# Kernel optimization log

Hardware: AMD Instinct MI355X
Metric: run time of the kernel (lower is better)

The kernel has to match this reference:

```python
import jax, jax.numpy as jnp
import numpy as np

N = 50000
E = 800000
IN_CH, CDK, EDGE_DIM = 40, 200, 10
HID, HEADS = 64, 4
NEG_SLOPE = 0.2
SM_EPS = 1e-16
BN_EPS = 1e-5


def _glorot(key, shape):
    fan = shape[0] + shape[-1]
    return jax.random.normal(key, shape, jnp.float32) * jnp.sqrt(2.0 / fan)


def setup_inputs() -> dict:
    key = jax.random.key(0)
    ks = iter(jax.random.split(key, 40))
    inp = {
        'x': jax.random.normal(next(ks), (N, IN_CH), jnp.float32),
        'cdk_desc': jax.random.normal(next(ks), (N, CDK), jnp.float32),
        'edge_src': jax.random.randint(next(ks), (E,), 0, N, jnp.int32),
        'edge_dst': jax.random.randint(next(ks), (E,), 0, N, jnp.int32),
        'edge_attr': jax.random.normal(next(ks), (E, EDGE_DIM), jnp.float32),
    }
    dims = [(IN_CH + CDK, HEADS, HID), (HID * HEADS, HEADS, HID), (HID * HEADS, 1, HID)]
    for i, (din, h, c) in enumerate(dims):
        inp[f'W{i}'] = _glorot(next(ks), (din, h * c))
        inp[f'as{i}'] = _glorot(next(ks), (h, c))
        inp[f'ad{i}'] = _glorot(next(ks), (h, c))
        inp[f'We{i}'] = _glorot(next(ks), (EDGE_DIM, h * c))
        inp[f'ae{i}'] = _glorot(next(ks), (h, c))
        inp[f'b{i}'] = jnp.zeros((h * c,), jnp.float32)
        inp[f'g{i}'] = jnp.ones((h * c,), jnp.float32)
        inp[f'be{i}'] = jnp.zeros((h * c,), jnp.float32)
    inp['linW'] = _glorot(next(ks), (HID, 1))
    inp['linB'] = jnp.zeros((1,), jnp.float32)
    return inp


def gat_conv(x, src, dst, ea, W, a_s, a_d, We, a_e, b, heads, c):
    # PyG GATConv: shared linear for src/dst, edge features, segment softmax.
    xp = (x @ W).reshape(N, heads, c)                 # [N,H,C]
    ep = (ea @ We).reshape(-1, heads, c)              # [Etot,H,C]
    al_s = (xp * a_s).sum(-1)                         # [N,H]
    al_d = (xp * a_d).sum(-1)                         # [N,H]
    al_e = (ep * a_e).sum(-1)                         # [Etot,H]
    alpha = jax.nn.leaky_relu(al_s[src] + al_d[dst] + al_e, NEG_SLOPE)
    m = jax.ops.segment_max(alpha, dst, num_segments=N)
    ex = jnp.exp(alpha - m[dst])
    den = jax.ops.segment_sum(ex, dst, num_segments=N)
    att = ex / (den[dst] + SM_EPS)                    # [Etot,H]
    out = jax.ops.segment_sum(xp[src] * att[:, :, None], dst, num_segments=N)
    return out.reshape(N, heads * c) + b


def batch_norm(x, g, be):
    mu = x.mean(0)
    var = x.var(0)
    return g * (x - mu) * jax.lax.rsqrt(var + BN_EPS) + be


def reference(x, cdk_desc, edge_src, edge_dst, edge_attr,
              W0, as0, ad0, We0, ae0, b0, g0, be0,
              W1, as1, ad1, We1, ae1, b1, g1, be1,
              W2, as2, ad2, We2, ae2, b2, g2, be2,
              linW, linB):
    # add self-loops once (PyG default add_self_loops=True, fill_value='mean')
    loop = jnp.arange(N, dtype=edge_src.dtype)
    src = jnp.concatenate([edge_src, loop])
    dst = jnp.concatenate([edge_dst, loop])
    ea_mean = edge_attr.mean(0)
    ea = jnp.concatenate([edge_attr, jnp.broadcast_to(ea_mean, (N, EDGE_DIM))], 0)

    h = jnp.concatenate([x, cdk_desc], axis=-1)
    layers = [
        (W0, as0, ad0, We0, ae0, b0, g0, be0, HEADS),
        (W1, as1, ad1, We1, ae1, b1, g1, be1, HEADS),
        (W2, as2, ad2, We2, ae2, b2, g2, be2, 1),
    ]
    for (W, a_s, a_d, We, a_e, b, g, be, heads) in layers:
        h = gat_conv(h, src, dst, ea, W, a_s, a_d, We, a_e, b, heads, HID)
        h = batch_norm(h, g, be)
        h = jax.nn.elu(h)
        # dropout is identity in eval mode
    out = h @ linW + linB
    return jax.nn.sigmoid(out).squeeze(-1)
```

## Files before the change

kernel.cpp:

```cpp
#include <hip/hip_runtime.h>
#include <math.h>

#define NNODES 50000
#define NEDGES 800000
#define ETOT   (NNODES + NEDGES)
#define EDIM   10
#define SMEPS  1e-16f
#define BNEPS  1e-5f
#define NSLOPE 0.2f

#define SCANB  ((NNODES + 255) / 256)
#define EASUMB 256
#define BNB    256

typedef _Float16 f16;
typedef f16 f16x8 __attribute__((ext_vector_type(8)));
typedef f16 f16x4 __attribute__((ext_vector_type(4)));
typedef float f32x4 __attribute__((ext_vector_type(4)));


__global__ void k_deg(const int* __restrict__ edst, int* __restrict__ deg) {
    int e = blockIdx.x * blockDim.x + threadIdx.x;
    if (e >= ETOT) return;
    int d = (e < NEDGES) ? edst[e] : (e - NEDGES);
    atomicAdd(&deg[d], 1);
}

__global__ void k_easum(const float* __restrict__ ea, float* __restrict__ part) {
    float acc[EDIM];
#pragma unroll
    for (int d = 0; d < EDIM; ++d) acc[d] = 0.f;
    int tid = blockIdx.x * blockDim.x + threadIdx.x;
    const int np = NEDGES / 2;
    for (int p = tid; p < np; p += gridDim.x * blockDim.x) {
        const float4* q = (const float4*)&ea[(long)p * 20];
        float4 v0 = q[0], v1 = q[1], v2 = q[2], v3 = q[3], v4 = q[4];
        acc[0] += v0.x + v2.z;
        acc[1] += v0.y + v2.w;
        acc[2] += v0.z + v3.x;
        acc[3] += v0.w + v3.y;
        acc[4] += v1.x + v3.z;
        acc[5] += v1.y + v3.w;
        acc[6] += v1.z + v4.x;
        acc[7] += v1.w + v4.y;
        acc[8] += v2.x + v4.z;
        acc[9] += v2.y + v4.w;
    }
    __shared__ float sm[256];
    for (int d = 0; d < EDIM; ++d) {
        sm[threadIdx.x] = acc[d];
        __syncthreads();
        for (int s = 128; s > 0; s >>= 1) {
            if (threadIdx.x < s) sm[threadIdx.x] += sm[threadIdx.x + s];
            __syncthreads();
        }
        if (threadIdx.x == 0) part[blockIdx.x * EDIM + d] = sm[0];
        __syncthreads();
    }
}

__global__ void k_scan1(const int* __restrict__ deg, int* __restrict__ off,
                        int* __restrict__ partials) {
    __shared__ int sm[256];
    int t = threadIdx.x;
    int i = blockIdx.x * 256 + t;
    int v = (i < NNODES) ? deg[i] : 0;
    sm[t] = v;
    __syncthreads();
    int val = v;
    for (int d = 1; d < 256; d <<= 1) {
        int tv = (t >= d) ? sm[t - d] : 0;
        __syncthreads();
        val += tv;
        sm[t] = val;
        __syncthreads();
    }
    if (i < NNODES) off[i] = val - v;
    if (t == 255) partials[blockIdx.x] = val;
}

__global__ void k_scan2(int* __restrict__ partials, int* __restrict__ off) {
    __shared__ int sm[256];
    int t = threadIdx.x;
    int v = (t < SCANB) ? partials[t] : 0;
    sm[t] = v;
    __syncthreads();
    int val = v;
    for (int d = 1; d < 256; d <<= 1) {
        int tv = (t >= d) ? sm[t - d] : 0;
        __syncthreads();
        val += tv;
        sm[t] = val;
        __syncthreads();
    }
    if (t < SCANB) partials[t] = val - v;
    if (t == 255) off[NNODES] = ETOT;
}

__global__ void k_scan3(int* __restrict__ off, const int* __restrict__ partials) {
    int i = blockIdx.x * 256 + threadIdx.x;
    if (i < NNODES) off[i] += partials[blockIdx.x];
}

__global__ void k_scatter(const int* __restrict__ esrc, const int* __restrict__ edst,
                          const int* __restrict__ off, int* __restrict__ cursor,
                          int* __restrict__ csr_src, int* __restrict__ perm) {
    int e = blockIdx.x * blockDim.x + threadIdx.x;
    if (e >= ETOT) return;
    int s, d;
    if (e < NEDGES) { s = esrc[e]; d = edst[e]; }
    else            { s = d = e - NEDGES; }
    int pos  = atomicAdd(&cursor[d], 1);
    int slot = off[d] + pos;
    csr_src[slot] = s;
    perm[e] = slot;
}

__global__ void k_concat_h(const float* __restrict__ x, const float* __restrict__ cdk,
                           f16* __restrict__ out) {
    int i = blockIdx.x * blockDim.x + threadIdx.x;
    if (i >= NNODES * 256) return;
    int n = i >> 8, j = i & 255;
    float v = (j < 40) ? x[n * 40 + j] : (j < 240) ? cdk[n * 200 + (j - 40)] : 0.f;
    out[i] = (f16)v;
}

__global__ void k_wcvt_all(const float* __restrict__ W0, const float* __restrict__ W1,
                           const float* __restrict__ W2, f16* __restrict__ Wt0,
                           f16* __restrict__ Wt1, f16* __restrict__ Wt2) {
    int i = blockIdx.x * blockDim.x + threadIdx.x;
    const float* W; f16* Wt; int K, NC, j;
    if (i < 65536)       { W = W0; Wt = Wt0; K = 240; NC = 256; j = i; }
    else if (i < 131072) { W = W1; Wt = Wt1; K = 256; NC = 256; j = i - 65536; }
    else if (i < 147456) { W = W2; Wt = Wt2; K = 256; NC = 64;  j = i - 131072; }
    else return;
    int n = j >> 8, k = j & 255;
    Wt[j] = (k < K) ? (f16)W[k * NC + n] : (f16)0.f;
}

#define GM_LDS 40
__global__ __launch_bounds__(256) void k_gemm_h(const f16* __restrict__ A,
                                                const f16* __restrict__ Bt,
                                                f16* __restrict__ C,
                                                const float* __restrict__ a_s,
                                                const float* __restrict__ a_d,
                                                float* __restrict__ als,
                                                float* __restrict__ ald,
                                                int M, int NC, int H) {
    __shared__ f16 As[128 * GM_LDS];
    __shared__ f16 Bs[64 * GM_LDS];
    const int t    = threadIdx.x;
    const int w    = t >> 6;
    const int lane = t & 63;
    const int row0 = blockIdx.x * 128;
    const int col0 = blockIdx.y * 64;

    const int ar = t >> 1;
    const int ak = (t & 1) * 16;
    const int bn = t >> 2;
    const int bk = (t & 3) * 8;

    const int l16 = lane & 15;
    const int kg  = lane >> 4;

    f32x4 acc[2][4];
#pragma unroll
    for (int i = 0; i < 2; ++i)
#pragma unroll
        for (int j = 0; j < 4; ++j) acc[i][j] = {0.f, 0.f, 0.f, 0.f};

    for (int k0 = 0; k0 < 256; k0 += 32) {
        f16x8 av0, av1;
#pragma unroll
        for (int i = 0; i < 8; ++i) { av0[i] = (f16)0.f; av1[i] = (f16)0.f; }
        if (row0 + ar < M) {
            const f16* ap = &A[(long)(row0 + ar) * 256 + k0 + ak];
            av0 = *(const f16x8*)ap;
            av1 = *(const f16x8*)(ap + 8);
        }
        *(f16x8*)&As[ar * GM_LDS + ak]     = av0;
        *(f16x8*)&As[ar * GM_LDS + ak + 8] = av1;
        f16x8 bv = *(const f16x8*)&Bt[(long)(col0 + bn) * 256 + k0 + bk];
        *(f16x8*)&Bs[bn * GM_LDS + bk] = bv;
        __syncthreads();

        f16x8 afr[2], bfr[4];
#pragma unroll
        for (int mi = 0; mi < 2; ++mi)
            afr[mi] = *(const f16x8*)&As[(w * 32 + mi * 16 + l16) * GM_LDS + kg * 8];
#pragma unroll
        for (int ni = 0; ni < 4; ++ni)
            bfr[ni] = *(const f16x8*)&Bs[(ni * 16 + l16) * GM_LDS + kg * 8];
#pragma unroll
        for (int mi = 0; mi < 2; ++mi)
#pragma unroll
            for (int ni = 0; ni < 4; ++ni)
                acc[mi][ni] = __builtin_amdgcn_mfma_f32_16x16x32_f16(
                    afr[mi], bfr[ni], acc[mi][ni], 0, 0, 0);
        __syncthreads();
    }

#pragma unroll
    for (int mi = 0; mi < 2; ++mi)
#pragma unroll
        for (int ni = 0; ni < 4; ++ni)
#pragma unroll
            for (int j = 0; j < 4; ++j) {
                int r = row0 + w * 32 + mi * 16 + kg * 4 + j;
                if (r < M) C[(long)r * NC + col0 + ni * 16 + l16] = (f16)acc[mi][ni][j];
            }

    const int hidx = blockIdx.y;
    float asv[4], adv[4];
#pragma unroll
    for (int ni = 0; ni < 4; ++ni) {
        asv[ni] = a_s[hidx * 64 + ni * 16 + l16];
        adv[ni] = a_d[hidx * 64 + ni * 16 + l16];
    }
#pragma unroll
    for (int mi = 0; mi < 2; ++mi)
#pragma unroll
        for (int j = 0; j < 4; ++j) {
            float ps = acc[mi][0][j] * asv[0] + acc[mi][1][j] * asv[1]
                     + acc[mi][2][j] * asv[2] + acc[mi][3][j] * asv[3];
            float pd = acc[mi][0][j] * adv[0] + acc[mi][1][j] * adv[1]
                     + acc[mi][2][j] * adv[2] + acc[mi][3][j] * adv[3];
#pragma unroll
            for (int o = 1; o < 16; o <<= 1) {
                ps += __shfl_xor(ps, o);
                pd += __shfl_xor(pd, o);
            }
            int r = row0 + w * 32 + mi * 16 + kg * 4 + j;
            if (l16 == 0 && r < M) {
                als[(long)r * H + hidx] = ps;
                ald[(long)r * H + hidx] = pd;
            }
        }
}

__global__ void k_ve_all(const float* __restrict__ We0, const float* __restrict__ ae0,
                         const float* __restrict__ We1, const float* __restrict__ ae1,
                         const float* __restrict__ We2, const float* __restrict__ ae2,
                         const float* __restrict__ eapart,
                         float* __restrict__ VeAll, float* __restrict__ laAll) {
    int l = blockIdx.x;
    const float* We = (l == 0) ? We0 : (l == 1) ? We1 : We2;
    const float* ae = (l == 0) ? ae0 : (l == 1) ? ae1 : ae2;
    int H = (l == 2) ? 1 : 4;
    float* Ve = VeAll + l * 48;
    float* la = laAll + l * 4;
    int t = threadIdx.x;

    float ac[EDIM];
#pragma unroll
    for (int d = 0; d < EDIM; ++d) ac[d] = 0.f;
    for (int r = t; r < EASUMB; r += 64) {
#pragma unroll
        for (int d = 0; d < EDIM; ++d) ac[d] += eapart[r * EDIM + d];
    }
#pragma unroll
    for (int o = 1; o < 64; o <<= 1) {
#pragma unroll
        for (int d = 0; d < EDIM; ++d) ac[d] += __shfl_xor(ac[d], o);
    }

    if (t < EDIM * H) {
        int d = t / H, h = t % H;
        float s = 0.f;
        for (int c = 0; c < 64; ++c) s += We[d * (H * 64) + h * 64 + c] * ae[h * 64 + c];
        Ve[d * H + h] = s;
    }
    __syncthreads();
    if (t < H) {
        float s = 0.f;
        for (int d = 0; d < EDIM; ++d) s += (ac[d] * (1.0f / NEDGES)) * Ve[d * H + t];
        la[t] = s;
    }
}

template <int H>
__global__ void k_edge(const float* __restrict__ ea, const int* __restrict__ esrc,
                       const int* __restrict__ edst, const float* __restrict__ als,
                       const float* __restrict__ ald, const float* __restrict__ Ve,
                       const float* __restrict__ loop_al, const int* __restrict__ perm,
                       f16* __restrict__ alpha) {
    int e = blockIdx.x * blockDim.x + threadIdx.x;
    if (e >= ETOT) return;
    int s, d;
    float ale[H];
    if (e < NEDGES) {
        s = esrc[e]; d = edst[e];
#pragma unroll
        for (int h = 0; h < H; ++h) ale[h] = 0.f;
#pragma unroll
        for (int dd = 0; dd < EDIM; ++dd) {
            float v = ea[(long)e * EDIM + dd];
#pragma unroll
            for (int h = 0; h < H; ++h) ale[h] = fmaf(v, Ve[dd * H + h], ale[h]);
        }
    } else {
        s = d = e - NEDGES;
#pragma unroll
        for (int h = 0; h < H; ++h) ale[h] = loop_al[h];
    }
    int slot = perm[e];
#pragma unroll
    for (int h = 0; h < H; ++h) {
        float a = als[s * H + h] + ald[d * H + h] + ale[h];
        a = (a > 0.f) ? a : NSLOPE * a;
        alpha[(long)slot * H + h] = (f16)a;
    }
}

template <int H>
__global__ __launch_bounds__(256) void k_agg(const f16* __restrict__ xp,
                                             const f16* __restrict__ alpha,
                                             const int* __restrict__ off,
                                             const int* __restrict__ csr_src,
                                             f16* __restrict__ out) {
    int gw   = (blockIdx.x * blockDim.x + threadIdx.x) >> 6;
    int lane = threadIdx.x & 63;
    if (gw >= NNODES) return;
    int o0 = off[gw], o1 = off[gw + 1];

    if constexpr (H == 4) {
        constexpr int T = 4;
        int h  = lane >> 4;
        int il = lane & 15;
        int glane = lane & 48;

        float av[T];
        int   idx[T];
        float mx = -INFINITY;
#pragma unroll
        for (int t = 0; t < T; ++t) {
            int s = o0 + t * 16 + il;
            bool ok = (s < o1);
            float a = ok ? (float)alpha[(long)s * 4 + h] : -INFINITY;
            idx[t] = ok ? csr_src[s] : 0;
            av[t] = a;
            mx = fmaxf(mx, a);
        }
        for (int s = o0 + T * 16 + il; s < o1; s += 16)
            mx = fmaxf(mx, (float)alpha[(long)s * 4 + h]);
#pragma unroll
        for (int o = 1; o < 16; o <<= 1) mx = fmaxf(mx, __shfl_xor(mx, o));

        float den = 0.f;
#pragma unroll
        for (int t = 0; t < T; ++t) {
            float e = expf(av[t] - mx);
            av[t] = e;
            den += e;
        }
        for (int s = o0 + T * 16 + il; s < o1; s += 16)
            den += expf((float)alpha[(long)s * 4 + h] - mx);
#pragma unroll
        for (int o = 1; o < 16; o <<= 1) den += __shfl_xor(den, o);
        float di = 1.0f / (den + SMEPS);

        float4 acc0 = make_float4(0.f, 0.f, 0.f, 0.f);
        float4 acc1 = make_float4(0.f, 0.f, 0.f, 0.f);
#pragma unroll
        for (int t = 0; t < T; ++t) {
            int base = o0 + t * 16;
            if (base >= o1) break;
            int cnt = min(16, o1 - base);
            int j = 0;
            for (; j + 4 <= cnt; j += 4) {
                float w0 = __shfl(av[t],  glane + j,     64);
                int  sn0 = __shfl(idx[t], glane + j,     64);
                float w1 = __shfl(av[t],  glane + j + 1, 64);
                int  sn1 = __shfl(idx[t], glane + j + 1, 64);
                float w2 = __shfl(av[t],  glane + j + 2, 64);
                int  sn2 = __shfl(idx[t], glane + j + 2, 64);
                float w3 = __shfl(av[t],  glane + j + 3, 64);
                int  sn3 = __shfl(idx[t], glane + j + 3, 64);
                f16x4 x0 = *(const f16x4*)&xp[(long)sn0 * 256 + lane * 4];
                f16x4 x1 = *(const f16x4*)&xp[(long)sn1 * 256 + lane * 4];
                f16x4 x2 = *(const f16x4*)&xp[(long)sn2 * 256 + lane * 4];
                f16x4 x3 = *(const f16x4*)&xp[(long)sn3 * 256 + lane * 4];
                acc0.x = fmaf(w0, (float)x0[0], acc0.x);
                acc0.y = fmaf(w0, (float)x0[1], acc0.y);
                acc0.z = fmaf(w0, (float)x0[2], acc0.z);
                acc0.w = fmaf(w0, (float)x0[3], acc0.w);
                acc1.x = fmaf(w1, (float)x1[0], acc1.x);
                acc1.y = fmaf(w1, (float)x1[1], acc1.y);
                acc1.z = fmaf(w1, (float)x1[2], acc1.z);
                acc1.w = fmaf(w1, (float)x1[3], acc1.w);
                acc0.x = fmaf(w2, (float)x2[0], acc0.x);
                acc0.y = fmaf(w2, (float)x2[1], acc0.y);
                acc0.z = fmaf(w2, (float)x2[2], acc0.z);
                acc0.w = fmaf(w2, (float)x2[3], acc0.w);
                acc1.x = fmaf(w3, (float)x3[0], acc1.x);
                acc1.y = fmaf(w3, (float)x3[1], acc1.y);
                acc1.z = fmaf(w3, (float)x3[2], acc1.z);
                acc1.w = fmaf(w3, (float)x3[3], acc1.w);
            }
            for (; j < cnt; ++j) {
                float w  = __shfl(av[t],  glane + j, 64);
                int   sn = __shfl(idx[t], glane + j, 64);
                f16x4 xh = *(const f16x4*)&xp[(long)sn * 256 + lane * 4];
                acc0.x = fmaf(w, (float)xh[0], acc0.x);
                acc0.y = fmaf(w, (float)xh[1], acc0.y);
                acc0.z = fmaf(w, (float)xh[2], acc0.z);
                acc0.w = fmaf(w, (float)xh[3], acc0.w);
            }
        }
        for (int s = o0 + T * 16; s < o1; ++s) {
            float w  = expf((float)alpha[(long)s * 4 + h] - mx);
            int   sn = csr_src[s];
            f16x4 xh = *(const f16x4*)&xp[(long)sn * 256 + lane * 4];
            acc0.x = fmaf(w, (float)xh[0], acc0.x);
            acc0.y = fmaf(w, (float)xh[1], acc0.y);
            acc0.z = fmaf(w, (float)xh[2], acc0.z);
            acc0.w = fmaf(w, (float)xh[3], acc0.w);
        }
        f16x4 o4 = {(f16)((acc0.x + acc1.x) * di), (f16)((acc0.y + acc1.y) * di),
                    (f16)((acc0.z + acc1.z) * di), (f16)((acc0.w + acc1.w) * di)};
        *(f16x4*)&out[(long)gw * 256 + lane * 4] = o4;
    } else {
        constexpr int T = 2;
        float av[T];
        int   idx[T];
        float mx = -INFINITY;
#pragma unroll
        for (int t = 0; t < T; ++t) {
            int s = o0 + t * 64 + lane;
            bool ok = (s < o1);
            float a = ok ? (float)alpha[s] : -INFINITY;
            idx[t] = ok ? csr_src[s] : 0;
            av[t] = a;
            mx = fmaxf(mx, a);
        }
        for (int s = o0 + T * 64 + lane; s < o1; s += 64)
            mx = fmaxf(mx, (float)alpha[s]);
#pragma unroll
        for (int o = 1; o < 64; o <<= 1) mx = fmaxf(mx, __shfl_xor(mx, o));

        float den = 0.f;
#pragma unroll
        for (int t = 0; t < T; ++t) {
            float e = expf(av[t] - mx);
            av[t] = e;
            den += e;
        }
        for (int s = o0 + T * 64 + lane; s < o1; s += 64)
            den += expf((float)alpha[s] - mx);
#pragma unroll
        for (int o = 1; o < 64; o <<= 1) den += __shfl_xor(den, o);
        float di = 1.0f / (den + SMEPS);

        float acc0 = 0.f, acc1 = 0.f;
#pragma unroll
        for (int t = 0; t < T; ++t) {
            int base = o0 + t * 64;
            if (base >= o1) break;
            int c2 = min(64, o1 - base);
            int j = 0;
            for (; j + 4 <= c2; j += 4) {
                float w0 = __shfl(av[t],  j,     64);
                int  sn0 = __shfl(idx[t], j,     64);
                float w1 = __shfl(av[t],  j + 1, 64);
                int  sn1 = __shfl(idx[t], j + 1, 64);
                float w2 = __shfl(av[t],  j + 2, 64);
                int  sn2 = __shfl(idx[t], j + 2, 64);
                float w3 = __shfl(av[t],  j + 3, 64);
                int  sn3 = __shfl(idx[t], j + 3, 64);
                float x0 = (float)xp[(long)sn0 * 64 + lane];
                float x1 = (float)xp[(long)sn1 * 64 + lane];
                float x2 = (float)xp[(long)sn2 * 64 + lane];
                float x3 = (float)xp[(long)sn3 * 64 + lane];
                acc0 = fmaf(w0, x0, acc0);
                acc1 = fmaf(w1, x1, acc1);
                acc0 = fmaf(w2, x2, acc0);
                acc1 = fmaf(w3, x3, acc1);
            }
            for (; j < c2; ++j) {
                float w  = __shfl(av[t],  j, 64);
                int   sn = __shfl(idx[t], j, 64);
                acc0 = fmaf(w, (float)xp[(long)sn * 64 + lane], acc0);
            }
        }
        for (int s = o0 + T * 64; s < o1; ++s) {
            float w  = expf((float)alpha[s] - mx);
            int   sn = csr_src[s];
            acc0 = fmaf(w, (float)xp[(long)sn * 64 + lane], acc0);
        }
        out[(long)gw * 64 + lane] = (f16)((acc0 + acc1) * di);
    }
}

__global__ void k_bnstats(const f16* __restrict__ x, int width,
                          float* __restrict__ s1p, float* __restrict__ s2p) {
    __shared__ float sa[256], sb[256];
    int col  = threadIdx.x % width;
    int rsub = threadIdx.x / width;
    int rpb  = 256 / width;
    float a = 0.f, b = 0.f;
    for (int r = blockIdx.x * rpb + rsub; r < NNODES; r += gridDim.x * rpb) {
        float v = (float)x[(long)r * width + col];
        a += v; b += v * v;
    }
    if (rpb == 1) {
        s1p[blockIdx.x * width + col] = a;
        s2p[blockIdx.x * width + col] = b;
    } else {
        sa[threadIdx.x] = a;
        sb[threadIdx.x] = b;
        __syncthreads();
        if (rsub == 0) {
            for (int k = 1; k < rpb; ++k) {
                a += sa[col + k * width];
                b += sb[col + k * width];
            }
            s1p[blockIdx.x * width + col] = a;
            s2p[blockIdx.x * width + col] = b;
        }
    }
}

__global__ void k_bnfin(const float* __restrict__ s1p, const float* __restrict__ s2p,
                        const float* __restrict__ g, const float* __restrict__ be,
                        int width, float* __restrict__ scale, float* __restrict__ shift) {
    int c = threadIdx.x;
    if (c >= width) return;
    float s1 = 0.f, s2 = 0.f;
    for (int k = 0; k < BNB; ++k) {
        s1 += s1p[k * width + c];
        s2 += s2p[k * width + c];
    }
    float mu  = s1 * (1.0f / NNODES);
    float var = s2 * (1.0f / NNODES) - mu * mu;
    float sc  = g[c] * rsqrtf(var + BNEPS);
    scale[c] = sc;
    shift[c] = be[c] - mu * sc;
}

__global__ void k_bnelu_h(const f16* __restrict__ xin, f16* __restrict__ xout,
                          const float* __restrict__ scale, const float* __restrict__ shift,
                          int width) {
    long i = (long)(blockIdx.x * blockDim.x + threadIdx.x);
    long total = (long)NNODES * width;
    if (i * 4 >= total) return;
    f16x4 v4 = *(const f16x4*)&xin[i * 4];
    int c = (int)((i * 4) % width);
    float4 sc = *(const float4*)&scale[c];
    float4 sh = *(const float4*)&shift[c];
    float y0 = (float)v4[0] * sc.x + sh.x;
    float y1 = (float)v4[1] * sc.y + sh.y;
    float y2 = (float)v4[2] * sc.z + sh.z;
    float y3 = (float)v4[3] * sc.w + sh.w;
    y0 = (y0 > 0.f) ? y0 : expm1f(y0);
    y1 = (y1 > 0.f) ? y1 : expm1f(y1);
    y2 = (y2 > 0.f) ? y2 : expm1f(y2);
    y3 = (y3 > 0.f) ? y3 : expm1f(y3);
    f16x4 o = {(f16)y0, (f16)y1, (f16)y2, (f16)y3};
    *(f16x4*)&xout[i * 4] = o;
}

__global__ __launch_bounds__(256) void k_final(const f16* __restrict__ h,
                                               const float* __restrict__ linW,
                                               const float* __restrict__ linB,
                                               float* __restrict__ out) {
    int gw   = (blockIdx.x * blockDim.x + threadIdx.x) >> 6;
    int lane = threadIdx.x & 63;
    if (gw >= NNODES) return;
    float v = (float)h[(long)gw * 64 + lane] * linW[lane];
    for (int o = 32; o > 0; o >>= 1) v += __shfl_xor(v, o);
    if (lane == 0) out[gw] = 1.0f / (1.0f + expf(-(v + linB[0])));
}

extern "C" void kernel_launch(void* const* d_in, const int* in_sizes, int n_in,
                              void* d_out, int out_size, void* d_ws, size_t ws_size,
                              hipStream_t stream) {
    (void)in_sizes; (void)n_in; (void)out_size; (void)ws_size;
    const float* x    = (const float*)d_in[0];
    const float* cdk  = (const float*)d_in[1];
    const int*   esrc = (const int*)d_in[2];
    const int*   edst = (const int*)d_in[3];
    const float* ea   = (const float*)d_in[4];
    const float* W[3]   = {(const float*)d_in[5],  (const float*)d_in[13], (const float*)d_in[21]};
    const float* as_[3] = {(const float*)d_in[6],  (const float*)d_in[14], (const float*)d_in[22]};
    const float* ad_[3] = {(const float*)d_in[7],  (const float*)d_in[15], (const float*)d_in[23]};
    const float* We_[3] = {(const float*)d_in[8],  (const float*)d_in[16], (const float*)d_in[24]};
    const float* ae_[3] = {(const float*)d_in[9],  (const float*)d_in[17], (const float*)d_in[25]};
    const float* g_[3]  = {(const float*)d_in[11], (const float*)d_in[19], (const float*)d_in[27]};
    const float* be_[3] = {(const float*)d_in[12], (const float*)d_in[20], (const float*)d_in[28]};
    const float* linW = (const float*)d_in[29];
    const float* linB = (const float*)d_in[30];
    float* out = (float*)d_out;

    char* base = (char*)d_ws;
    size_t p = 0;
    auto alloc = [&](size_t bytes) -> void* {
        void* r = base + p;
        p = (p + bytes + 255) & ~(size_t)255;
        return r;
    };
    int*   deg     = (int*)alloc((size_t)NNODES * 4);
    int*   cursor  = (int*)alloc((size_t)NNODES * 4);
    size_t zero_bytes = p;
    int*   off     = (int*)alloc((size_t)(NNODES + 1) * 4);
    int*   partials= (int*)alloc((size_t)SCANB * 4);
    float* eapart  = (float*)alloc((size_t)EASUMB * EDIM * 4);
    float* s1p     = (float*)alloc((size_t)BNB * 256 * 4);
    float* s2p     = (float*)alloc((size_t)BNB * 256 * 4);
    int*   csr_src = (int*)alloc((size_t)ETOT * 4);
    int*   perm    = (int*)alloc((size_t)ETOT * 4);
    f16*   alpha   = (f16*)alloc((size_t)ETOT * 4 * 2);
    float* als     = (float*)alloc((size_t)NNODES * 4 * 4);
    float* ald     = (float*)alloc((size_t)NNODES * 4 * 4);
    float* VeAll   = (float*)alloc((size_t)3 * 48 * 4);
    float* laAll   = (float*)alloc((size_t)3 * 4 * 4);
    float* scale   = (float*)alloc(256 * 4);
    float* shift   = (float*)alloc(256 * 4);
    f16*   Wt[3];
    Wt[0]          = (f16*)alloc((size_t)256 * 256 * 2);
    Wt[1]          = (f16*)alloc((size_t)256 * 256 * 2);
    Wt[2]          = (f16*)alloc((size_t)64 * 256 * 2);
    f16*   bufA_h  = (f16*)alloc((size_t)NNODES * 256 * 2);
    f16*   bufXp_h = (f16*)alloc((size_t)NNODES * 256 * 2);
    f16*   bufC_h  = (f16*)alloc((size_t)NNODES * 256 * 2);

    hipMemsetAsync(base, 0, zero_bytes, stream);

    int eb = (ETOT + 255) / 256;
    k_deg<<<eb, 256, 0, stream>>>(edst, deg);
    k_easum<<<EASUMB, 256, 0, stream>>>(ea, eapart);
    k_scan1<<<SCANB, 256, 0, stream>>>(deg, off, partials);
    k_scan2<<<1, 256, 0, stream>>>(partials, off);
    k_scan3<<<SCANB, 256, 0, stream>>>(off, partials);
    k_scatter<<<eb, 256, 0, stream>>>(esrc, edst, off, cursor, csr_src, perm);
    k_concat_h<<<(NNODES * 256 + 255) / 256, 256, 0, stream>>>(x, cdk, bufA_h);
    k_wcvt_all<<<576, 256, 0, stream>>>(W[0], W[1], W[2], Wt[0], Wt[1], Wt[2]);
    k_ve_all<<<3, 64, 0, stream>>>(We_[0], ae_[0], We_[1], ae_[1], We_[2], ae_[2],
                                   eapart, VeAll, laAll);

    const int nodeblocks = (NNODES * 64) / 256;
    const int mblocks = (NNODES + 127) / 128;

    for (int l = 0; l < 3; ++l) {
        const int H  = (l == 2) ? 1 : 4;
        const int NC = H * 64;
        const float* Ve  = VeAll + l * 48;
        const float* la  = laAll + l * 4;
        dim3 gg(mblocks, NC / 64);
        k_gemm_h<<<gg, 256, 0, stream>>>(bufA_h, Wt[l], bufXp_h,
                                         as_[l], ad_[l], als, ald, NNODES, NC, H);
        if (H == 4) {
            k_edge<4><<<eb, 256, 0, stream>>>(ea, esrc, edst, als, ald, Ve, la, perm, alpha);
            k_agg<4><<<nodeblocks, 256, 0, stream>>>(bufXp_h, alpha, off, csr_src, bufC_h);
        } else {
            k_edge<1><<<eb, 256, 0, stream>>>(ea, esrc, edst, als, ald, Ve, la, perm, alpha);
            k_agg<1><<<nodeblocks, 256, 0, stream>>>(bufXp_h, alpha, off, csr_src, bufC_h);
        }
        k_bnstats<<<BNB, 256, 0, stream>>>(bufC_h, NC, s1p, s2p);
        k_bnfin<<<1, 256, 0, stream>>>(s1p, s2p, g_[l], be_[l], NC, scale, shift);
        k_bnelu_h<<<(NNODES * NC / 4 + 255) / 256, 256, 0, stream>>>(bufC_h, bufA_h, scale, shift, NC);
    }
    k_final<<<nodeblocks, 256, 0, stream>>>(bufA_h, linW, linB, out);
}
```

Baseline: 631.8 us.

## Replace CSR build with fixed-capacity per-node edge slots plus overflow list

```diff
diff --git a/kernel.cpp b/kernel.cpp
--- a/kernel.cpp
+++ b/kernel.cpp
@@ -9,21 +9,35 @@
 #define BNEPS  1e-5f
 #define NSLOPE 0.2f
 
-#define SCANB  ((NNODES + 255) / 256)
 #define EASUMB 256
 #define BNB    256
+#define CAP    64
 
 typedef _Float16 f16;
 typedef f16 f16x8 __attribute__((ext_vector_type(8)));
 typedef f16 f16x4 __attribute__((ext_vector_type(4)));
 typedef float f32x4 __attribute__((ext_vector_type(4)));
 
-
-__global__ void k_deg(const int* __restrict__ edst, int* __restrict__ deg) {
+__global__ void k_place(const int* __restrict__ esrc, const int* __restrict__ edst,
+                        int* __restrict__ deg, int* __restrict__ csr_src,
+                        int* __restrict__ perm, int* __restrict__ ovf_cnt,
+                        int* __restrict__ ovf_src, int* __restrict__ ovf_dst) {
     int e = blockIdx.x * blockDim.x + threadIdx.x;
     if (e >= ETOT) return;
-    int d = (e < NEDGES) ? edst[e] : (e - NEDGES);
-    atomicAdd(&deg[d], 1);
+    int s, d;
+    if (e < NEDGES) { s = esrc[e]; d = edst[e]; }
+    else            { s = d = e - NEDGES; }
+    int pos = atomicAdd(&deg[d], 1);
+    if (pos < CAP) {
+        int slot = d * CAP + pos;
+        csr_src[slot] = s;
+        perm[e] = slot;
+    } else {
+        int k = atomicAdd(ovf_cnt, 1);
+        ovf_src[k] = s;
+        ovf_dst[k] = d;
+        perm[e] = -1 - k;
+    }
 }
 
 __global__ void k_easum(const float* __restrict__ ea, float* __restrict__ part) {
@@ -59,63 +73,6 @@
     }
 }
 
-__global__ void k_scan1(const int* __restrict__ deg, int* __restrict__ off,
-                        int* __restrict__ partials) {
-    __shared__ int sm[256];
-    int t = threadIdx.x;
-    int i = blockIdx.x * 256 + t;
-    int v = (i < NNODES) ? deg[i] : 0;
-    sm[t] = v;
-    __syncthreads();
-    int val = v;
-    for (int d = 1; d < 256; d <<= 1) {
-        int tv = (t >= d) ? sm[t - d] : 0;
-        __syncthreads();
-        val += tv;
-        sm[t] = val;
-        __syncthreads();
-    }
-    if (i < NNODES) off[i] = val - v;
-    if (t == 255) partials[blockIdx.x] = val;
-}
-
-__global__ void k_scan2(int* __restrict__ partials, int* __restrict__ off) {
-    __shared__ int sm[256];
-    int t = threadIdx.x;
-    int v = (t < SCANB) ? partials[t] : 0;
-    sm[t] = v;
-    __syncthreads();
-    int val = v;
-    for (int d = 1; d < 256; d <<= 1) {
-        int tv = (t >= d) ? sm[t - d] : 0;
-        __syncthreads();
-        val += tv;
-        sm[t] = val;
-        __syncthreads();
-    }
-    if (t < SCANB) partials[t] = val - v;
-    if (t == 255) off[NNODES] = ETOT;
-}
-
-__global__ void k_scan3(int* __restrict__ off, const int* __restrict__ partials) {
-    int i = blockIdx.x * 256 + threadIdx.x;
-    if (i < NNODES) off[i] += partials[blockIdx.x];
-}
-
-__global__ void k_scatter(const int* __restrict__ esrc, const int* __restrict__ edst,
-                          const int* __restrict__ off, int* __restrict__ cursor,
-                          int* __restrict__ csr_src, int* __restrict__ perm) {
-    int e = blockIdx.x * blockDim.x + threadIdx.x;
-    if (e >= ETOT) return;
-    int s, d;
-    if (e < NEDGES) { s = esrc[e]; d = edst[e]; }
-    else            { s = d = e - NEDGES; }
-    int pos  = atomicAdd(&cursor[d], 1);
-    int slot = off[d] + pos;
-    csr_src[slot] = s;
-    perm[e] = slot;
-}
-
 __global__ void k_concat_h(const float* __restrict__ x, const float* __restrict__ cdk,
                            f16* __restrict__ out) {
     int i = blockIdx.x * blockDim.x + threadIdx.x;
@@ -283,7 +240,7 @@
                        const int* __restrict__ edst, const float* __restrict__ als,
                        const float* __restrict__ ald, const float* __restrict__ Ve,
                        const float* __restrict__ loop_al, const int* __restrict__ perm,
-                       f16* __restrict__ alpha) {
+                       f16* __restrict__ alpha, f16* __restrict__ alpha_ovf) {
     int e = blockIdx.x * blockDim.x + threadIdx.x;
     if (e >= ETOT) return;
     int s, d;
@@ -304,24 +261,34 @@
         for (int h = 0; h < H; ++h) ale[h] = loop_al[h];
     }
     int slot = perm[e];
+    f16* dst = (slot >= 0) ? &alpha[(long)slot * H]
+                           : &alpha_ovf[(long)(-1 - slot) * H];
 #pragma unroll
     for (int h = 0; h < H; ++h) {
         float a = als[s * H + h] + ald[d * H + h] + ale[h];
         a = (a > 0.f) ? a : NSLOPE * a;
-        alpha[(long)slot * H + h] = (f16)a;
+        dst[h] = (f16)a;
     }
 }
 
 template <int H>
 __global__ __launch_bounds__(256) void k_agg(const f16* __restrict__ xp,
                                              const f16* __restrict__ alpha,
-                                             const int* __restrict__ off,
+                                             const int* __restrict__ deg,
                                              const int* __restrict__ csr_src,
+                                             const int* __restrict__ ovf_cnt,
+                                             const int* __restrict__ ovf_src,
+                                             const int* __restrict__ ovf_dst,
+                                             const f16* __restrict__ alpha_ovf,
                                              f16* __restrict__ out) {
     int gw   = (blockIdx.x * blockDim.x + threadIdx.x) >> 6;
     int lane = threadIdx.x & 63;
     if (gw >= NNODES) return;
-    int o0 = off[gw], o1 = off[gw + 1];
+    int dcount = deg[gw];
+    int cnt = min(dcount, CAP);
+    int o0 = gw * CAP;
+    int o1 = o0 + cnt;
+    bool ovf = (dcount > CAP);
 
     if constexpr (H == 4) {
         constexpr int T = 4;
@@ -341,10 +308,14 @@
             av[t] = a;
             mx = fmaxf(mx, a);
         }
-        for (int s = o0 + T * 16 + il; s < o1; s += 16)
-            mx = fmaxf(mx, (float)alpha[(long)s * 4 + h]);
 #pragma unroll
         for (int o = 1; o < 16; o <<= 1) mx = fmaxf(mx, __shfl_xor(mx, o));
+        if (ovf) {
+            int nov = *ovf_cnt;
+            for (int k = 0; k < nov; ++k)
+                if (ovf_dst[k] == gw)
+                    mx = fmaxf(mx, (float)alpha_ovf[(long)k * 4 + h]);
+        }
 
         float den = 0.f;
 #pragma unroll
@@ -353,21 +324,25 @@
             av[t] = e;
             den += e;
         }
-        for (int s = o0 + T * 16 + il; s < o1; s += 16)
-            den += expf((float)alpha[(long)s * 4 + h] - mx);
 #pragma unroll
         for (int o = 1; o < 16; o <<= 1) den += __shfl_xor(den, o);
+        if (ovf) {
+            int nov = *ovf_cnt;
+            for (int k = 0; k < nov; ++k)
+                if (ovf_dst[k] == gw)
+                    den += expf((float)alpha_ovf[(long)k * 4 + h] - mx);
+        }
         float di = 1.0f / (den + SMEPS);
 
         float4 acc0 = make_float4(0.f, 0.f, 0.f, 0.f);
         float4 acc1 = make_float4(0.f, 0.f, 0.f, 0.f);
 #pragma unroll
         for (int t = 0; t < T; ++t) {
-            int base = o0 + t * 16;
-            if (base >= o1) break;
-            int cnt = min(16, o1 - base);
+            int base = t * 16;
+            if (base >= cnt) break;
+            int c2 = min(16, cnt - base);
             int j = 0;
-            for (; j + 4 <= cnt; j += 4) {
+            for (; j + 4 <= c2; j += 4) {
                 float w0 = __shfl(av[t],  glane + j,     64);
                 int  sn0 = __shfl(idx[t], glane + j,     64);
                 float w1 = __shfl(av[t],  glane + j + 1, 64);
@@ -397,7 +372,7 @@
                 acc1.z = fmaf(w3, (float)x3[2], acc1.z);
                 acc1.w = fmaf(w3, (float)x3[3], acc1.w);
             }
-            for (; j < cnt; ++j) {
+            for (; j < c2; ++j) {
                 float w  = __shfl(av[t],  glane + j, 64);
                 int   sn = __shfl(idx[t], glane + j, 64);
                 f16x4 xh = *(const f16x4*)&xp[(long)sn * 256 + lane * 4];
@@ -407,85 +382,83 @@
                 acc0.w = fmaf(w, (float)xh[3], acc0.w);
             }
         }
-        for (int s = o0 + T * 16; s < o1; ++s) {
-            float w  = expf((float)alpha[(long)s * 4 + h] - mx);
-            int   sn = csr_src[s];
-            f16x4 xh = *(const f16x4*)&xp[(long)sn * 256 + lane * 4];
-            acc0.x = fmaf(w, (float)xh[0], acc0.x);
-            acc0.y = fmaf(w, (float)xh[1], acc0.y);
-            acc0.z = fmaf(w, (float)xh[2], acc0.z);
-            acc0.w = fmaf(w, (float)xh[3], acc0.w);
+        if (ovf) {
+            int nov = *ovf_cnt;
+            for (int k = 0; k < nov; ++k) {
+                if (ovf_dst[k] == gw) {
+                    float w  = expf((float)alpha_ovf[(long)k * 4 + h] - mx);
+                    int   sn = ovf_src[k];
+                    f16x4 xh = *(const f16x4*)&xp[(long)sn * 256 + lane * 4];
+                    acc0.x = fmaf(w, (float)xh[0], acc0.x);
+                    acc0.y = fmaf(w, (float)xh[1], acc0.y);
+                    acc0.z = fmaf(w, (float)xh[2], acc0.z);
+                    acc0.w = fmaf(w, (float)xh[3], acc0.w);
+                }
+            }
         }
         f16x4 o4 = {(f16)((acc0.x + acc1.x) * di), (f16)((acc0.y + acc1.y) * di),
                     (f16)((acc0.z + acc1.z) * di), (f16)((acc0.w + acc1.w) * di)};
         *(f16x4*)&out[(long)gw * 256 + lane * 4] = o4;
     } else {
-        constexpr int T = 2;
-        float av[T];
-        int   idx[T];
-        float mx = -INFINITY;
-#pragma unroll
-        for (int t = 0; t < T; ++t) {
-            int s = o0 + t * 64 + lane;
-            bool ok = (s < o1);
-            float a = ok ? (float)alpha[s] : -INFINITY;
-            idx[t] = ok ? csr_src[s] : 0;
-            av[t] = a;
-            mx = fmaxf(mx, a);
-        }
-        for (int s = o0 + T * 64 + lane; s < o1; s += 64)
-            mx = fmaxf(mx, (float)alpha[s]);
+        int s = o0 + lane;
+        bool ok = (lane < cnt);
+        float av0 = ok ? (float)alpha[s] : -INFINITY;
+        int   id0 = ok ? csr_src[s] : 0;
+        float mx = av0;
 #pragma unroll
         for (int o = 1; o < 64; o <<= 1) mx = fmaxf(mx, __shfl_xor(mx, o));
-
-        float den = 0.f;
-#pragma unroll
-        for (int t = 0; t < T; ++t) {
-            float e = expf(av[t] - mx);
-            av[t] = e;
-            den += e;
-        }
-        for (int s = o0 + T * 64 + lane; s < o1; s += 64)
-            den += expf((float)alpha[s] - mx);
+        if (ovf) {
+            int nov = *ovf_cnt;
+            for (int k = 0; k < nov; ++k)
+                if (ovf_dst[k] == gw)
+                    mx = fmaxf(mx, (float)alpha_ovf[k]);
+        }
+        float e0 = expf(av0 - mx);
+        float den = e0;
 #pragma unroll
         for (int o = 1; o < 64; o <<= 1) den += __shfl_xor(den, o);
+        if (ovf) {
+            int nov = *ovf_cnt;
+            for (int k = 0; k < nov; ++k)
+                if (ovf_dst[k] == gw)
+                    den += expf((float)alpha_ovf[k] - mx);
+        }
         float di = 1.0f / (den + SMEPS);
 
         float acc0 = 0.f, acc1 = 0.f;
-#pragma unroll
-        for (int t = 0; t < T; ++t) {
-            int base = o0 + t * 64;
-            if (base >= o1) break;
-            int c2 = min(64, o1 - base);
-            int j = 0;
-            for (; j + 4 <= c2; j += 4) {
-                float w0 = __shfl(av[t],  j,     64);
-                int  sn0 = __shfl(idx[t], j,     64);
-                float w1 = __shfl(av[t],  j + 1, 64);
-                int  sn1 = __shfl(idx[t], j + 1, 64);
-                float w2 = __shfl(av[t],  j + 2, 64);
-                int  sn2 = __shfl(idx[t], j + 2, 64);
-                float w3 = __shfl(av[t],  j + 3, 64);
-                int  sn3 = __shfl(idx[t], j + 3, 64);
-                float x0 = (float)xp[(long)sn0 * 64 + lane];
-                float x1 = (float)xp[(long)sn1 * 64 + lane];
-                float x2 = (float)xp[(long)sn2 * 64 + lane];
-                float x3 = (float)xp[(long)sn3 * 64 + lane];
-                acc0 = fmaf(w0, x0, acc0);
-                acc1 = fmaf(w1, x1, acc1);
-                acc0 = fmaf(w2, x2, acc0);
-                acc1 = fmaf(w3, x3, acc1);
-            }
-            for (; j < c2; ++j) {
-                float w  = __shfl(av[t],  j, 64);
-                int   sn = __shfl(idx[t], j, 64);
-                acc0 = fmaf(w, (float)xp[(long)sn * 64 + lane], acc0);
-            }
-        }
-        for (int s = o0 + T * 64; s < o1; ++s) {
-            float w  = expf((float)alpha[s] - mx);
-            int   sn = csr_src[s];
+        int j = 0;
+        for (; j + 4 <= cnt; j += 4) {
+            float w0 = __shfl(e0,  j,     64);
+            int  sn0 = __shfl(id0, j,     64);
+            float w1 = __shfl(e0,  j + 1, 64);
+            int  sn1 = __shfl(id0, j + 1, 64);
+            float w2 = __shfl(e0,  j + 2, 64);
+            int  sn2 = __shfl(id0, j + 2, 64);
+            float w3 = __shfl(e0,  j + 3, 64);
+            int  sn3 = __shfl(id0, j + 3, 64);
+            float x0 = (float)xp[(long)sn0 * 64 + lane];
+            float x1 = (float)xp[(long)sn1 * 64 + lane];
+            float x2 = (float)xp[(long)sn2 * 64 + lane];
+            float x3 = (float)xp[(long)sn3 * 64 + lane];
+            acc0 = fmaf(w0, x0, acc0);
+            acc1 = fmaf(w1, x1, acc1);
+            acc0 = fmaf(w2, x2, acc0);
+            acc1 = fmaf(w3, x3, acc1);
+        }
+        for (; j < cnt; ++j) {
+            float w  = __shfl(e0,  j, 64);
+            int   sn = __shfl(id0, j, 64);
             acc0 = fmaf(w, (float)xp[(long)sn * 64 + lane], acc0);
+        }
+        if (ovf) {
+            int nov = *ovf_cnt;
+            for (int k = 0; k < nov; ++k) {
+                if (ovf_dst[k] == gw) {
+                    float w  = expf((float)alpha_ovf[k] - mx);
+                    int   sn = ovf_src[k];
+                    acc0 = fmaf(w, (float)xp[(long)sn * 64 + lane], acc0);
+                }
+            }
         }
         out[(long)gw * 64 + lane] = (f16)((acc0 + acc1) * di);
     }
@@ -599,16 +572,17 @@
         return r;
     };
     int*   deg     = (int*)alloc((size_t)NNODES * 4);
-    int*   cursor  = (int*)alloc((size_t)NNODES * 4);
+    int*   ovf_cnt = (int*)alloc(4);
     size_t zero_bytes = p;
-    int*   off     = (int*)alloc((size_t)(NNODES + 1) * 4);
-    int*   partials= (int*)alloc((size_t)SCANB * 4);
     float* eapart  = (float*)alloc((size_t)EASUMB * EDIM * 4);
     float* s1p     = (float*)alloc((size_t)BNB * 256 * 4);
     float* s2p     = (float*)alloc((size_t)BNB * 256 * 4);
-    int*   csr_src = (int*)alloc((size_t)ETOT * 4);
+    int*   csr_src = (int*)alloc((size_t)NNODES * CAP * 4);
     int*   perm    = (int*)alloc((size_t)ETOT * 4);
-    f16*   alpha   = (f16*)alloc((size_t)ETOT * 4 * 2);
+    f16*   alpha   = (f16*)alloc((size_t)NNODES * CAP * 4 * 2);
+    int*   ovf_src = (int*)alloc((size_t)ETOT * 4);
+    int*   ovf_dst = (int*)alloc((size_t)ETOT * 4);
+    f16*   alpha_o = (f16*)alloc((size_t)ETOT * 4 * 2);
     float* als     = (float*)alloc((size_t)NNODES * 4 * 4);
     float* ald     = (float*)alloc((size_t)NNODES * 4 * 4);
     float* VeAll   = (float*)alloc((size_t)3 * 48 * 4);
@@ -626,12 +600,9 @@
     hipMemsetAsync(base, 0, zero_bytes, stream);
 
     int eb = (ETOT + 255) / 256;
-    k_deg<<<eb, 256, 0, stream>>>(edst, deg);
+    k_place<<<eb, 256, 0, stream>>>(esrc, edst, deg, csr_src, perm,
+                                    ovf_cnt, ovf_src, ovf_dst);
     k_easum<<<EASUMB, 256, 0, stream>>>(ea, eapart);
-    k_scan1<<<SCANB, 256, 0, stream>>>(deg, off, partials);
-    k_scan2<<<1, 256, 0, stream>>>(partials, off);
-    k_scan3<<<SCANB, 256, 0, stream>>>(off, partials);
-    k_scatter<<<eb, 256, 0, stream>>>(esrc, edst, off, cursor, csr_src, perm);
     k_concat_h<<<(NNODES * 256 + 255) / 256, 256, 0, stream>>>(x, cdk, bufA_h);
     k_wcvt_all<<<576, 256, 0, stream>>>(W[0], W[1], W[2], Wt[0], Wt[1], Wt[2]);
     k_ve_all<<<3, 64, 0, stream>>>(We_[0], ae_[0], We_[1], ae_[1], We_[2], ae_[2],
@@ -649,11 +620,17 @@
         k_gemm_h<<<gg, 256, 0, stream>>>(bufA_h, Wt[l], bufXp_h,
                                          as_[l], ad_[l], als, ald, NNODES, NC, H);
         if (H == 4) {
-            k_edge<4><<<eb, 256, 0, stream>>>(ea, esrc, edst, als, ald, Ve, la, perm, alpha);
-            k_agg<4><<<nodeblocks, 256, 0, stream>>>(bufXp_h, alpha, off, csr_src, bufC_h);
+            k_edge<4><<<eb, 256, 0, stream>>>(ea, esrc, edst, als, ald, Ve, la,
+                                              perm, alpha, alpha_o);
+            k_agg<4><<<nodeblocks, 256, 0, stream>>>(bufXp_h, alpha, deg, csr_src,
+                                                     ovf_cnt, ovf_src, ovf_dst,
+                                                     alpha_o, bufC_h);
         } else {
-            k_edge<1><<<eb, 256, 0, stream>>>(ea, esrc, edst, als, ald, Ve, la, perm, alpha);
-            k_agg<1><<<nodeblocks, 256, 0, stream>>>(bufXp_h, alpha, off, csr_src, bufC_h);
+            k_edge<1><<<eb, 256, 0, stream>>>(ea, esrc, edst, als, ald, Ve, la,
+                                              perm, alpha, alpha_o);
+            k_agg<1><<<nodeblocks, 256, 0, stream>>>(bufXp_h, alpha, deg, csr_src,
+                                                     ovf_cnt, ovf_src, ovf_dst,
+                                                     alpha_o, bufC_h);
         }
         k_bnstats<<<BNB, 256, 0, stream>>>(bufC_h, NC, s1p, s2p);
         k_bnfin<<<1, 256, 0, stream>>>(s1p, s2p, g_[l], be_[l], NC, scale, shift);
```

Result: faster. 582.5 us (-7.8%).
